# Kernel optimization log

Measured on AMD Instinct MI355X. Metric: run time of the kernel, lower is better.

Reference implementation:

```python
import jax, jax.numpy as jnp
import numpy as np

B, S, E = 4, 4096, 512
H, D = 8, 64
BS = 64
R = 3
FF = 2048
N = S // BS
NEG = -10000.0


def _ln(x, g, b):
    m = jnp.mean(x, -1, keepdims=True)
    v = jnp.mean((x - m) ** 2, -1, keepdims=True)
    return (x - m) * jax.lax.rsqrt(v + 1e-6) * g + b


def setup_inputs():
    key = jax.random.key(0)
    k = jax.random.split(key, 8)
    s = 0.02
    return {
        "inputs": jax.random.normal(k[0], (B, S, E), jnp.float32),
        "band_mask": jnp.ones((B, 1, N - 4, BS, 3 * BS), jnp.float32),
        "from_mask": jnp.ones((B, 1, S, 1), jnp.float32),
        "to_mask": jnp.ones((B, 1, 1, S), jnp.float32),
        "blocked_mask": jnp.ones((B, N, BS), jnp.float32),
        "Wq": jax.random.normal(k[1], (E, H, D), jnp.float32) * s,
        "bq": jnp.zeros((H, D), jnp.float32),
        "Wk": jax.random.normal(k[2], (E, H, D), jnp.float32) * s,
        "bk": jnp.zeros((H, D), jnp.float32),
        "Wv": jax.random.normal(k[3], (E, H, D), jnp.float32) * s,
        "bv": jnp.zeros((H, D), jnp.float32),
        "Wo": jax.random.normal(k[4], (H, D, E), jnp.float32) * s,
        "bo": jnp.zeros((E,), jnp.float32),
        "W1": jax.random.normal(k[5], (E, FF), jnp.float32) * s,
        "b1": jnp.zeros((FF,), jnp.float32),
        "W2": jax.random.normal(k[6], (FF, E), jnp.float32) * s,
        "b2": jnp.zeros((E,), jnp.float32),
        "g1": jnp.ones((E,), jnp.float32),
        "beta1": jnp.zeros((E,), jnp.float32),
        "g2": jnp.ones((E,), jnp.float32),
        "beta2": jnp.zeros((E,), jnp.float32),
        "rand_attn": jax.random.randint(k[7], (H, N - 2, R), 0, N, jnp.int32),
    }


def _forward(inputs, band_mask, from_mask, to_mask, blocked_mask, Wq, bq, Wk, bk, Wv, bv, Wo, bo, W1, b1, W2, b2, g1, beta1, g2, beta2, rand_attn):
    b, s, e = inputs.shape
    h, d = Wq.shape[1], Wq.shape[2]
    bs = blocked_mask.shape[2]
    n = s // bs
    r = rand_attn.shape[2]
    scale = d ** -0.5
    # qkv projections (Dense3d): [b,s,e] -> [b,h,s,d]
    q = jnp.einsum("bse,ehd->bhsd", inputs, Wq) + bq[None, :, None, :]
    kmat = jnp.einsum("bse,ehd->bhsd", inputs, Wk) + bk[None, :, None, :]
    vmat = jnp.einsum("bse,ehd->bhsd", inputs, Wv) + bv[None, :, None, :]
    qb = q.reshape(b, h, n, bs, d)
    kb = kmat.reshape(b, h, n, bs, d)
    vb = vmat.reshape(b, h, n, bs, d)
    # gather per-head random key/value blocks: [b,h,n-2,r*bs,d]
    hidx = jnp.arange(h)[:, None, None]
    gk = kb[:, hidx, rand_attn].reshape(b, h, n - 2, r * bs, d)
    gv = vb[:, hidx, rand_attn].reshape(b, h, n - 2, r * bs, d)
    gm = blocked_mask[:, rand_attn].reshape(b, h, n - 2, r * bs)
    rand_mask = jnp.einsum("blq,bhlk->bhlqk", blocked_mask[:, 1:-1], gm)
    # first query block: dense attention over all keys
    fp = jnp.einsum("bhqd,bhkd->bhqk", qb[:, :, 0], kmat) * scale + (1.0 - to_mask) * NEG
    fc = jnp.einsum("bhqk,bhkd->bhqd", jax.nn.softmax(fp, -1), vmat)
    # second query block: blocks [0,1,2,-1] + random blocks of row 1
    skm = jnp.concatenate([kb[:, :, 0], kb[:, :, 1], kb[:, :, 2], kb[:, :, -1], gk[:, :, 0]], 2)
    svm = jnp.concatenate([vb[:, :, 0], vb[:, :, 1], vb[:, :, 2], vb[:, :, -1], gv[:, :, 0]], 2)
    seq_pad = jnp.concatenate([to_mask[:, :, :, :3 * bs], to_mask[:, :, :, -bs:], jnp.ones((b, 1, 1, r * bs), to_mask.dtype)], 3)
    rand_pad = jnp.concatenate([jnp.ones((b, h, bs, 4 * bs), rand_mask.dtype), rand_mask[:, :, 0]], 3)
    sp = jnp.einsum("bhqd,bhkd->bhqk", qb[:, :, 1], skm) * scale + (1.0 - jnp.minimum(seq_pad, rand_pad)) * NEG
    sc = jnp.einsum("bhqk,bhkd->bhqd", jax.nn.softmax(sp, -1), svm)
    # middle blocks: sliding 3-block band + random + global first/last blocks
    mq = qb[:, :, 2:-2]  # [b,h,n-4,bs,d]
    ekm = jnp.concatenate([kb[:, :, 1:-3], kb[:, :, 2:-2], kb[:, :, 3:-1]], 3)  # [b,h,n-4,3bs,d]
    evm = jnp.concatenate([vb[:, :, 1:-3], vb[:, :, 2:-2], vb[:, :, 3:-1]], 3)
    inner = jnp.einsum("bhlqd,bhlkd->bhlqk", mq, ekm) * scale + (1.0 - band_mask) * NEG
    rbp = jnp.einsum("bhlqd,bhlkd->bhlqk", mq, gk[:, :, 1:-1]) * scale + (1.0 - rand_mask[:, :, 1:-1]) * NEG
    fbp = jnp.einsum("bhlqd,bhkd->bhlqk", mq, kb[:, :, 0]) * scale + (1.0 - to_mask[:, :, None, :, :bs]) * NEG
    lbp = jnp.einsum("bhlqd,bhkd->bhlqk", mq, kb[:, :, -1]) * scale + (1.0 - to_mask[:, :, None, :, -bs:]) * NEG
    ba = jax.nn.softmax(jnp.concatenate([fbp, inner, rbp, lbp], -1), -1)
    mc = (jnp.einsum("bhlqk,bhlkd->bhlqd", ba[..., bs:4 * bs], evm)
          + jnp.einsum("bhlqk,bhlkd->bhlqd", ba[..., 4 * bs:(4 + r) * bs], gv[:, :, 1:-1])
          + jnp.einsum("bhlqk,bhkd->bhlqd", ba[..., :bs], vb[:, :, 0])
          + jnp.einsum("bhlqk,bhkd->bhlqd", ba[..., -bs:], vb[:, :, -1]))
    # second-to-last query block
    slkm = jnp.concatenate([kb[:, :, 0], kb[:, :, -3], kb[:, :, -2], kb[:, :, -1], gk[:, :, -1]], 2)
    slvm = jnp.concatenate([vb[:, :, 0], vb[:, :, -3], vb[:, :, -2], vb[:, :, -1], gv[:, :, -1]], 2)
    sl_seq = jnp.concatenate([to_mask[:, :, :, :bs], to_mask[:, :, :, -3 * bs:], jnp.ones((b, 1, 1, r * bs), to_mask.dtype)], 3)
    sl_rand = jnp.concatenate([jnp.ones((b, h, bs, 4 * bs), rand_mask.dtype), rand_mask[:, :, -1]], 3)
    slp = jnp.einsum("bhqd,bhkd->bhqk", qb[:, :, -2], slkm) * scale + (1.0 - jnp.minimum(sl_seq, sl_rand)) * NEG
    slc = jnp.einsum("bhqk,bhkd->bhqd", jax.nn.softmax(slp, -1), slvm)
    # last query block: dense over all keys
    lp = jnp.einsum("bhqd,bhkd->bhqk", qb[:, :, -1], kmat) * scale + (1.0 - to_mask) * NEG
    lc = jnp.einsum("bhqk,bhkd->bhqd", jax.nn.softmax(lp, -1), vmat)
    ctx = jnp.concatenate([fc[:, :, None], sc[:, :, None], mc, slc[:, :, None], lc[:, :, None]], 2)
    ctx = ctx.reshape(b, h, s, d) * from_mask
    ctx = ctx.transpose(0, 2, 1, 3)  # [b,s,h,d]
    attn_out = jnp.einsum("bshd,hde->bse", ctx, Wo) + bo
    out1 = _ln(inputs + attn_out, g1, beta1)
    ffn = jnp.maximum(out1 @ W1 + b1, 0.0) @ W2 + b2
    return _ln(out1 + ffn, g2, beta2)


def reference(inputs, band_mask, from_mask, to_mask, blocked_mask, Wq, bq, Wk, bk, Wv, bv, Wo, bo, W1, b1, W2, b2, g1, beta1, g2, beta2, rand_attn):
    return _forward(inputs, band_mask, from_mask, to_mask, blocked_mask, Wq, bq, Wk, bk, Wv, bv, Wo, bo, W1, b1, W2, b2, g1, beta1, g2, beta2, rand_attn)
```

## Files before the change

### kernel.cpp

```cpp
#include <hip/hip_runtime.h>
#include <hip/hip_bf16.h>

typedef __bf16 bf16x8 __attribute__((ext_vector_type(8)));
typedef float f32x4 __attribute__((ext_vector_type(4)));

static constexpr size_t MB = 1024 * 1024;

__device__ __forceinline__ void gload16(const void* g, void* l) {
  __builtin_amdgcn_global_load_lds((const __attribute__((address_space(1))) unsigned int*)g,
                                   (__attribute__((address_space(3))) unsigned int*)l,
                                   16, 0, 0);
}

__device__ __forceinline__ unsigned short f2b(float x) {
  union { __hip_bfloat16 h; unsigned short u; } cv;
  cv.h = __float2bfloat16(x);
  return cv.u;
}

__global__ __launch_bounds__(256) void pack_k(
    const float* __restrict__ X,
    const float* __restrict__ Wq, const float* __restrict__ Wk, const float* __restrict__ Wv,
    const float* __restrict__ Wo, const float* __restrict__ W1, const float* __restrict__ W2,
    __hip_bfloat16* __restrict__ XB, __hip_bfloat16* __restrict__ WQKVT,
    __hip_bfloat16* __restrict__ WOT, __hip_bfloat16* __restrict__ W1T,
    __hip_bfloat16* __restrict__ W2T)
{
  unsigned int i = blockIdx.x * 256u + threadIdx.x;
  if (i < 8388608u) { XB[i] = __float2bfloat16(X[i]); return; }
  i -= 8388608u;
  if (i < 786432u) {
    unsigned int n = i >> 9, k = i & 511u, which = n >> 9, hd = n & 511u;
    const float* W = (which == 0) ? Wq : (which == 1) ? Wk : Wv;
    WQKVT[i] = __float2bfloat16(W[k * 512u + hd]);
    return;
  }
  i -= 786432u;
  if (i < 262144u) {
    unsigned int e = i >> 9, hd = i & 511u;
    WOT[i] = __float2bfloat16(Wo[hd * 512u + e]);
    return;
  }
  i -= 262144u;
  if (i < 1048576u) {
    unsigned int f = i >> 9, e = i & 511u;
    W1T[i] = __float2bfloat16(W1[e * 2048u + f]);
    return;
  }
  i -= 1048576u;
  {
    unsigned int e = i >> 11, f = i & 2047u;
    W2T[i] = __float2bfloat16(W2[f * 512u + e]);
  }
}

template<int EPI>
__global__ __launch_bounds__(256) void gemm_k(
    const __hip_bfloat16* __restrict__ A,
    const __hip_bfloat16* __restrict__ Bt,
    int M, int N, int K,
    const float* __restrict__ bias0, const float* __restrict__ bias1, const float* __restrict__ bias2,
    void* __restrict__ o0, void* __restrict__ o1, void* __restrict__ o2)
{
  __shared__ __align__(16) char lA[128 * 64 * 2];
  __shared__ __align__(16) char lB[128 * 64 * 2];
  const int tid = threadIdx.x;
  const int wv = tid >> 6, ln = tid & 63;
  const int g = ln >> 4, q16 = ln & 15;
  const int mT = M >> 7;
  const int bm = blockIdx.x % mT, bn = blockIdx.x / mT;
  const int row0 = bm << 7, col0 = bn << 7;
  const int wm = wv >> 1, wn = wv & 1;
  const int ktn = K >> 6;

  f32x4 acc[4][4] = {};

  for (int kt = 0; kt < ktn; ++kt) {
    #pragma unroll
    for (int c4 = 0; c4 < 4; ++c4) {
      int c = wv * 4 + c4;
      int o = c * 1024 + ln * 16;
      int r = o >> 7;
      int slot = (o >> 4) & 7;
      int koff = kt * 64 + ((slot ^ (r & 7)) << 3);
      gload16(A + (size_t)(row0 + r) * K + koff, lA + c * 1024);
      gload16(Bt + (size_t)(col0 + r) * K + koff, lB + c * 1024);
    }
    __syncthreads();
    #pragma unroll
    for (int ks = 0; ks < 2; ++ks) {
      bf16x8 af[4], bfr[4];
      #pragma unroll
      for (int m = 0; m < 4; ++m) {
        int r = wm * 64 + m * 16 + q16;
        af[m] = *(const bf16x8*)(lA + r * 128 + (((4 * ks + g) ^ (r & 7)) << 4));
      }
      #pragma unroll
      for (int n = 0; n < 4; ++n) {
        int r = wn * 64 + n * 16 + q16;
        bfr[n] = *(const bf16x8*)(lB + r * 128 + (((4 * ks + g) ^ (r & 7)) << 4));
      }
      #pragma unroll
      for (int m = 0; m < 4; ++m) {
        #pragma unroll
        for (int n = 0; n < 4; ++n) {
          acc[m][n] = __builtin_amdgcn_mfma_f32_16x16x32_bf16(af[m], bfr[n], acc[m][n], 0, 0, 0);
        }
      }
    }
    __syncthreads();
  }

  #pragma unroll
  for (int m = 0; m < 4; ++m) {
    int rowb = row0 + wm * 64 + m * 16 + g * 4;
    #pragma unroll
    for (int n = 0; n < 4; ++n) {
      int col = col0 + wn * 64 + n * 16 + q16;
      f32x4 v = acc[m][n];
      if constexpr (EPI == 0) {
        int which = col >> 9, hd = col & 511;
        int hh = hd >> 6, dd = hd & 63;
        float bb = ((which == 0) ? bias0 : (which == 1) ? bias1 : bias2)[hd];
        if (which == 2) {
          int b_ = rowb >> 12, s0 = rowb & 4095;
          unsigned int lo = (unsigned)f2b(v[0] + bb) | ((unsigned)f2b(v[1] + bb) << 16);
          unsigned int hi = (unsigned)f2b(v[2] + bb) | ((unsigned)f2b(v[3] + bb) << 16);
          uint2 pv; pv.x = lo; pv.y = hi;
          *(uint2*)((char*)o2 + (((size_t)(b_ * 8 + hh) * 64 + dd) * 4096 + s0) * 2) = pv;
        } else {
          __hip_bfloat16* base = (__hip_bfloat16*)((which == 0) ? o0 : o1);
          #pragma unroll
          for (int r = 0; r < 4; ++r) {
            int rowg = rowb + r;
            int b_ = rowg >> 12, s = rowg & 4095;
            base[((size_t)(b_ * 8 + hh) * 4096 + s) * 64 + dd] = __float2bfloat16(v[r] + bb);
          }
        }
      } else {
        float bb = bias0[col];
        __hip_bfloat16* O = (__hip_bfloat16*)o0;
        #pragma unroll
        for (int r = 0; r < 4; ++r) {
          float x = v[r] + bb;
          if constexpr (EPI == 2) x = fmaxf(x, 0.f);
          O[(size_t)(rowb + r) * N + col] = __float2bfloat16(x);
        }
      }
    }
  }
}

#define NMID 1984
__global__ __launch_bounds__(256) void attn_k(
    const __hip_bfloat16* __restrict__ QB,
    const __hip_bfloat16* __restrict__ KB,
    const __hip_bfloat16* __restrict__ VT,
    const int* __restrict__ rand_attn,
    __hip_bfloat16* __restrict__ CTX,
    float* __restrict__ EOT,
    float* __restrict__ EML)
{
  __shared__ __align__(16) char lK[4][8192];
  __shared__ __align__(16) char lV[4][8192];
  __shared__ __align__(16) char lP[4][2816];

  const int tid = threadIdx.x;
  const int wv = tid >> 6, ln = tid & 63;
  const int g = ln >> 4, q16 = ln & 15;

  const bool edge = (int)blockIdx.x >= NMID;
  int bh, l, nk, split = 0, chunk = 0;
  int r0 = 0, r1 = 0, r2 = 0;
  if (!edge) {
    bh = blockIdx.x / 62;
    l = 1 + blockIdx.x % 62;
    nk = (l == 1 || l == 62) ? 7 : 8;
    const int* rp = rand_attn + ((bh & 7) * 62 + (l - 1)) * 3;
    r0 = rp[0]; r1 = rp[1]; r2 = rp[2];
  } else {
    chunk = (int)blockIdx.x - NMID;
    split = chunk & 7;
    int be = chunk >> 3;
    bh = be >> 1;
    l = (be & 1) ? 63 : 0;
    nk = 8;
  }

  auto kbof = [&](int t) -> int {
    if (edge) return split * 8 + t;
    if (t == 0) return 0;
    if (t >= 4) return (t == 4) ? r0 : (t == 5) ? r1 : (t == 6) ? r2 : 63;
    if (l == 1) return (t == 3) ? 63 : t;
    return l - 2 + t;
  };

  const __hip_bfloat16* Kbase = KB + ((size_t)bh << 18);
  const __hip_bfloat16* Vbase = VT + ((size_t)bh << 18);

  auto stage = [&](int t) {
    int kb = kbof(t);
    char* dK = lK[t & 3];
    char* dV = lV[t & 3];
    #pragma unroll
    for (int cc = 0; cc < 2; ++cc) {
      int c = wv * 2 + cc;
      int o = c * 1024 + ln * 16;
      int r = o >> 7;
      int slot = (o >> 4) & 7;
      int sw8 = (slot ^ (r & 7)) << 3;
      gload16(Kbase + ((size_t)(kb * 64 + r) << 6) + sw8, dK + c * 1024);
      gload16(Vbase + ((size_t)r << 12) + kb * 64 + sw8, dV + c * 1024);
    }
  };

  const size_t sq = (size_t)bh * 4096 + l * 64 + wv * 16 + q16;
  bf16x8 qreg0 = *(const bf16x8*)(QB + sq * 64 + g * 8);
  bf16x8 qreg1 = *(const bf16x8*)(QB + sq * 64 + 32 + g * 8);

  f32x4 ot[4] = {};
  float l_part = 0.f;
  constexpr float C = 0.18033688011112042f;

  auto compute = [&](int t) {
    const char* bK = lK[t & 3];
    const char* bV = lV[t & 3];
    f32x4 st[4];
    #pragma unroll
    for (int m = 0; m < 4; ++m) {
      int r = m * 16 + q16;
      bf16x8 kf0 = *(const bf16x8*)(bK + r * 128 + ((g ^ (r & 7)) << 4));
      bf16x8 kf1 = *(const bf16x8*)(bK + r * 128 + (((4 + g) ^ (r & 7)) << 4));
      f32x4 z = {};
      st[m] = __builtin_amdgcn_mfma_f32_16x16x32_bf16(kf0, qreg0, z, 0, 0, 0);
      st[m] = __builtin_amdgcn_mfma_f32_16x16x32_bf16(kf1, qreg1, st[m], 0, 0, 0);
    }
    #pragma unroll
    for (int m = 0; m < 4; ++m) {
      #pragma unroll
      for (int r = 0; r < 4; ++r) {
        float p = __builtin_amdgcn_exp2f(st[m][r] * C);
        st[m][r] = p;
        l_part += p;
      }
    }
    #pragma unroll
    for (int m = 0; m < 4; ++m) {
      unsigned int lo = (unsigned)f2b(st[m][0]) | ((unsigned)f2b(st[m][1]) << 16);
      unsigned int hi = (unsigned)f2b(st[m][2]) | ((unsigned)f2b(st[m][3]) << 16);
      uint2 pv; pv.x = lo; pv.y = hi;
      *(uint2*)(lP[wv] + q16 * 176 + 32 * m + 8 * g) = pv;
    }
    asm volatile("s_waitcnt lgkmcnt(0)" ::: "memory");
    __builtin_amdgcn_sched_barrier(0);
    #pragma unroll
    for (int ks = 0; ks < 2; ++ks) {
      bf16x8 pb = *(const bf16x8*)(lP[wv] + q16 * 176 + 64 * ks + 16 * g);
      #pragma unroll
      for (int m = 0; m < 4; ++m) {
        int r = m * 16 + q16;
        bf16x8 vf = *(const bf16x8*)(bV + r * 128 + (((4 * ks + g) ^ (r & 7)) << 4));
        ot[m] = __builtin_amdgcn_mfma_f32_16x16x32_bf16(vf, pb, ot[m], 0, 0, 0);
      }
    }
  };

  stage(0); stage(1); stage(2);

  int t = 0;
  for (; t + 3 < nk; ++t) {
    asm volatile("s_waitcnt vmcnt(8)" ::: "memory");
    __builtin_amdgcn_s_barrier();
    __builtin_amdgcn_sched_barrier(0);
    stage(t + 3);
    compute(t);
  }
  asm volatile("s_waitcnt vmcnt(8)" ::: "memory");
  __builtin_amdgcn_s_barrier();
  __builtin_amdgcn_sched_barrier(0);
  compute(t); ++t;
  asm volatile("s_waitcnt vmcnt(4)" ::: "memory");
  __builtin_amdgcn_s_barrier();
  __builtin_amdgcn_sched_barrier(0);
  compute(t); ++t;
  asm volatile("s_waitcnt vmcnt(0)" ::: "memory");
  __builtin_amdgcn_s_barrier();
  __builtin_amdgcn_sched_barrier(0);
  compute(t);

  float lsum = l_part;
  lsum += __shfl_xor(lsum, 16);
  lsum += __shfl_xor(lsum, 32);

  if (!edge) {
    int b = bh >> 3, h = bh & 7;
    float inv = 1.f / lsum;
    size_t crow = ((size_t)b * 4096 + l * 64 + wv * 16 + q16) * 512 + h * 64;
    #pragma unroll
    for (int m = 0; m < 4; ++m) {
      int d0 = 16 * m + 4 * g;
      unsigned int lo = (unsigned)f2b(ot[m][0] * inv) | ((unsigned)f2b(ot[m][1] * inv) << 16);
      unsigned int hi = (unsigned)f2b(ot[m][2] * inv) | ((unsigned)f2b(ot[m][3] * inv) << 16);
      uint2 pv; pv.x = lo; pv.y = hi;
      *(uint2*)((char*)CTX + (crow + d0) * 2) = pv;
    }
  } else {
    int qg = wv * 16 + q16;
    float* O = EOT + (size_t)chunk * 4096;
    #pragma unroll
    for (int m = 0; m < 4; ++m) {
      #pragma unroll
      for (int r = 0; r < 4; ++r)
        O[(16 * m + 4 * g + r) * 64 + qg] = ot[m][r];
    }
    if (g == 0) EML[(size_t)chunk * 64 + qg] = lsum;
  }
}

__global__ __launch_bounds__(256) void attn_combine_k(
    const float* __restrict__ EOT, const float* __restrict__ EML,
    __hip_bfloat16* __restrict__ CTX)
{
  const int be = blockIdx.x;
  const int bh = be >> 1, e = be & 1, b = bh >> 3, h = bh & 7;
  const int q = threadIdx.x & 63, dgrp = threadIdx.x >> 6;

  float denom = 0.f;
  #pragma unroll
  for (int s = 0; s < 8; ++s) denom += EML[(size_t)(be * 8 + s) * 64 + q];
  float inv = 1.f / denom;

  const size_t srow = (size_t)b * 4096 + (e ? 4032 : 0) + q;
  #pragma unroll
  for (int dd = 0; dd < 16; ++dd) {
    int d = dgrp * 16 + dd;
    float acc = 0.f;
    #pragma unroll
    for (int s = 0; s < 8; ++s)
      acc += EOT[(size_t)(be * 8 + s) * 4096 + d * 64 + q];
    CTX[srow * 512 + h * 64 + d] = __float2bfloat16(acc * inv);
  }
}

template<typename TX, typename TY, bool OUTF>
__global__ __launch_bounds__(256) void ln_k(
    const TX* __restrict__ X, const TY* __restrict__ Y,
    const float* __restrict__ gamma, const float* __restrict__ beta,
    float* __restrict__ outF, __hip_bfloat16* __restrict__ outB)
{
  const int wv = threadIdx.x >> 6, ln = threadIdx.x & 63;
  const size_t row = (size_t)blockIdx.x * 4 + wv;
  float v[8];
  {
    const TX* xr = X + row * 512 + ln * 8;
    const TY* yr = Y + row * 512 + ln * 8;
    if constexpr (sizeof(TX) == 4) {
      float4 a0 = *(const float4*)xr, a1 = *(const float4*)(xr + 4);
      v[0]=a0.x; v[1]=a0.y; v[2]=a0.z; v[3]=a0.w; v[4]=a1.x; v[5]=a1.y; v[6]=a1.z; v[7]=a1.w;
    } else {
      bf16x8 a = *(const bf16x8*)xr;
      #pragma unroll
      for (int i = 0; i < 8; ++i) v[i] = (float)a[i];
    }
    if constexpr (sizeof(TY) == 4) {
      float4 b0 = *(const float4*)yr, b1 = *(const float4*)(yr + 4);
      v[0]+=b0.x; v[1]+=b0.y; v[2]+=b0.z; v[3]+=b0.w; v[4]+=b1.x; v[5]+=b1.y; v[6]+=b1.z; v[7]+=b1.w;
    } else {
      bf16x8 bv_ = *(const bf16x8*)yr;
      #pragma unroll
      for (int i = 0; i < 8; ++i) v[i] += (float)bv_[i];
    }
  }
  float s = 0.f;
  #pragma unroll
  for (int i = 0; i < 8; ++i) s += v[i];
  #pragma unroll
  for (int o = 1; o < 64; o <<= 1) s += __shfl_xor(s, o);
  float mean = s * (1.f / 512.f);
  float sq = 0.f;
  #pragma unroll
  for (int i = 0; i < 8; ++i) { float d = v[i] - mean; sq += d * d; }
  #pragma unroll
  for (int o = 1; o < 64; o <<= 1) sq += __shfl_xor(sq, o);
  float rs = rsqrtf(sq * (1.f / 512.f) + 1e-6f);
  float og[8];
  #pragma unroll
  for (int i = 0; i < 8; ++i)
    og[i] = (v[i] - mean) * rs * gamma[ln * 8 + i] + beta[ln * 8 + i];
  if constexpr (OUTF) {
    float4 o0; o0.x = og[0]; o0.y = og[1]; o0.z = og[2]; o0.w = og[3];
    float4 o1; o1.x = og[4]; o1.y = og[5]; o1.z = og[6]; o1.w = og[7];
    *(float4*)(outF + row * 512 + ln * 8) = o0;
    *(float4*)(outF + row * 512 + ln * 8 + 4) = o1;
  } else {
    unsigned int w0 = (unsigned)f2b(og[0]) | ((unsigned)f2b(og[1]) << 16);
    unsigned int w1 = (unsigned)f2b(og[2]) | ((unsigned)f2b(og[3]) << 16);
    unsigned int w2 = (unsigned)f2b(og[4]) | ((unsigned)f2b(og[5]) << 16);
    unsigned int w3 = (unsigned)f2b(og[6]) | ((unsigned)f2b(og[7]) << 16);
    uint2 p0; p0.x = w0; p0.y = w1;
    uint2 p1; p1.x = w2; p1.y = w3;
    *(uint2*)((char*)outB + (row * 512 + ln * 8) * 2) = p0;
    *(uint2*)((char*)outB + (row * 512 + ln * 8 + 4) * 2) = p1;
  }
}

extern "C" void kernel_launch(void* const* d_in, const int* in_sizes, int n_in,
                              void* d_out, int out_size, void* d_ws, size_t ws_size,
                              hipStream_t stream)
{
  (void)in_sizes; (void)n_in; (void)out_size; (void)ws_size;
  const float* X   = (const float*)d_in[0];
  const float* Wq  = (const float*)d_in[5];
  const float* bq  = (const float*)d_in[6];
  const float* Wk  = (const float*)d_in[7];
  const float* bk  = (const float*)d_in[8];
  const float* Wv  = (const float*)d_in[9];
  const float* bv  = (const float*)d_in[10];
  const float* Wo  = (const float*)d_in[11];
  const float* bo  = (const float*)d_in[12];
  const float* W1  = (const float*)d_in[13];
  const float* b1  = (const float*)d_in[14];
  const float* W2  = (const float*)d_in[15];
  const float* b2  = (const float*)d_in[16];
  const float* g1  = (const float*)d_in[17];
  const float* be1 = (const float*)d_in[18];
  const float* g2  = (const float*)d_in[19];
  const float* be2 = (const float*)d_in[20];
  const int*   ra  = (const int*)d_in[21];

  char* ws = (char*)d_ws;
  __hip_bfloat16* WQKVT = (__hip_bfloat16*)(ws + 0 * MB);
  __hip_bfloat16* WOT   = (__hip_bfloat16*)(ws + 2 * MB);
  __hip_bfloat16* W1T   = (__hip_bfloat16*)(ws + 3 * MB);
  __hip_bfloat16* W2T   = (__hip_bfloat16*)(ws + 5 * MB);
  __hip_bfloat16* XB    = (__hip_bfloat16*)(ws + 8 * MB);
  float*          EOT   = (float*)(ws + 8 * MB);
  float*          EML   = (float*)(ws + 16 * MB);
  __hip_bfloat16* QB    = (__hip_bfloat16*)(ws + 24 * MB);
  __hip_bfloat16* KBp   = (__hip_bfloat16*)(ws + 40 * MB);
  __hip_bfloat16* VTp   = (__hip_bfloat16*)(ws + 56 * MB);
  __hip_bfloat16* CTX   = (__hip_bfloat16*)(ws + 72 * MB);
  __hip_bfloat16* AOB   = (__hip_bfloat16*)(ws + 88 * MB);
  __hip_bfloat16* O1B   = (__hip_bfloat16*)(ws + 104 * MB);
  __hip_bfloat16* F2B   = (__hip_bfloat16*)(ws + 120 * MB);
  __hip_bfloat16* H1    = (__hip_bfloat16*)(ws + 24 * MB);

  pack_k<<<dim3(45056), dim3(256), 0, stream>>>(X, Wq, Wk, Wv, Wo, W1, W2,
                                                XB, WQKVT, WOT, W1T, W2T);
  gemm_k<0><<<dim3(128 * 12), dim3(256), 0, stream>>>(XB, WQKVT, 16384, 1536, 512,
                                                      bq, bk, bv, QB, KBp, VTp);
  attn_k<<<dim3(NMID + 512), dim3(256), 0, stream>>>(QB, KBp, VTp, ra, CTX, EOT, EML);
  attn_combine_k<<<dim3(64), dim3(256), 0, stream>>>(EOT, EML, CTX);
  gemm_k<1><<<dim3(128 * 4), dim3(256), 0, stream>>>(CTX, WOT, 16384, 512, 512,
                                                     bo, nullptr, nullptr, AOB, nullptr, nullptr);
  ln_k<float, __hip_bfloat16, false><<<dim3(4096), dim3(256), 0, stream>>>(
      X, AOB, g1, be1, nullptr, O1B);
  gemm_k<2><<<dim3(128 * 16), dim3(256), 0, stream>>>(O1B, W1T, 16384, 2048, 512,
                                                      b1, nullptr, nullptr, H1, nullptr, nullptr);
  gemm_k<1><<<dim3(128 * 4), dim3(256), 0, stream>>>(H1, W2T, 16384, 512, 2048,
                                                     b2, nullptr, nullptr, F2B, nullptr, nullptr);
  ln_k<__hip_bfloat16, __hip_bfloat16, true><<<dim3(4096), dim3(256), 0, stream>>>(
      O1B, F2B, g2, be2, (float*)d_out, nullptr);
}
```

Measured before the change: 264.3 us.

## Tile-transpose weight packing and split attention keys across two wave groups

The pack kernel now converts X with vectorized 8-element loads and stores, and transposes the weights through a shared-memory 64x64 tile so that both reads and writes are coalesced. The attention kernel doubles its block to 512 threads. Two wave groups each handle half of the key rows of every 64-key block, and their partial outputs and row sums are reduced through LDS at the end. The K/V pipeline drops from four buffers to two, waiting on vmcnt(0) each step. This trades load prefetch depth for more waves per block and adds an extra barrier plus an LDS reduction.

```diff
diff --git a/kernel.cpp b/kernel.cpp
--- a/kernel.cpp
+++ b/kernel.cpp
@@ -18,7 +18,7 @@
   return cv.u;
 }
 
-__global__ __launch_bounds__(256) void pack_k(
+__global__ __launch_bounds__(256) void pt_k(
     const float* __restrict__ X,
     const float* __restrict__ Wq, const float* __restrict__ Wk, const float* __restrict__ Wv,
     const float* __restrict__ Wo, const float* __restrict__ W1, const float* __restrict__ W2,
@@ -26,31 +26,41 @@
     __hip_bfloat16* __restrict__ WOT, __hip_bfloat16* __restrict__ W1T,
     __hip_bfloat16* __restrict__ W2T)
 {
-  unsigned int i = blockIdx.x * 256u + threadIdx.x;
-  if (i < 8388608u) { XB[i] = __float2bfloat16(X[i]); return; }
-  i -= 8388608u;
-  if (i < 786432u) {
-    unsigned int n = i >> 9, k = i & 511u, which = n >> 9, hd = n & 511u;
-    const float* W = (which == 0) ? Wq : (which == 1) ? Wk : Wv;
-    WQKVT[i] = __float2bfloat16(W[k * 512u + hd]);
+  __shared__ float tile[64][65];
+  const int bid = blockIdx.x, tid = threadIdx.x;
+  if (bid < 4096) {
+    size_t i = (size_t)bid * 2048 + tid * 8;
+    float4 a0 = *(const float4*)(X + i);
+    float4 a1 = *(const float4*)(X + i + 4);
+    unsigned int w0 = (unsigned)f2b(a0.x) | ((unsigned)f2b(a0.y) << 16);
+    unsigned int w1 = (unsigned)f2b(a0.z) | ((unsigned)f2b(a0.w) << 16);
+    unsigned int w2 = (unsigned)f2b(a1.x) | ((unsigned)f2b(a1.y) << 16);
+    unsigned int w3 = (unsigned)f2b(a1.z) | ((unsigned)f2b(a1.w) << 16);
+    uint4 p; p.x = w0; p.y = w1; p.z = w2; p.w = w3;
+    *(uint4*)(XB + i) = p;
     return;
   }
-  i -= 786432u;
-  if (i < 262144u) {
-    unsigned int e = i >> 9, hd = i & 511u;
-    WOT[i] = __float2bfloat16(Wo[hd * 512u + e]);
-    return;
-  }
-  i -= 262144u;
-  if (i < 1048576u) {
-    unsigned int f = i >> 9, e = i & 511u;
-    W1T[i] = __float2bfloat16(W1[e * 2048u + f]);
-    return;
-  }
-  i -= 1048576u;
-  {
-    unsigned int e = i >> 11, f = i & 2047u;
-    W2T[i] = __float2bfloat16(W2[f * 512u + e]);
+  int tb = bid - 4096;
+  const float* in; __hip_bfloat16* out; int R, C, tt;
+  if (tb < 64)       { in = Wq; out = WQKVT;          R = 512;  C = 512;  tt = tb; }
+  else if (tb < 128) { in = Wk; out = WQKVT + 262144; R = 512;  C = 512;  tt = tb - 64; }
+  else if (tb < 192) { in = Wv; out = WQKVT + 524288; R = 512;  C = 512;  tt = tb - 128; }
+  else if (tb < 256) { in = Wo; out = WOT;            R = 512;  C = 512;  tt = tb - 192; }
+  else if (tb < 512) { in = W1; out = W1T;            R = 512;  C = 2048; tt = tb - 256; }
+  else               { in = W2; out = W2T;            R = 2048; C = 512;  tt = tb - 512; }
+  const int ct = C >> 6;
+  const int r0 = (tt / ct) << 6, c0 = (tt % ct) << 6;
+  const int tx = tid & 63, ty = tid >> 6;
+  #pragma unroll
+  for (int j = 0; j < 16; ++j) {
+    int r = ty * 16 + j;
+    tile[r][tx] = in[(size_t)(r0 + r) * C + c0 + tx];
+  }
+  __syncthreads();
+  #pragma unroll
+  for (int j = 0; j < 16; ++j) {
+    int c = ty * 16 + j;
+    out[(size_t)(c0 + c) * R + r0 + tx] = __float2bfloat16(tile[tx][c]);
   }
 }
 
@@ -152,7 +162,7 @@
 }
 
 #define NMID 1984
-__global__ __launch_bounds__(256) void attn_k(
+__global__ __launch_bounds__(512) void attn_k(
     const __hip_bfloat16* __restrict__ QB,
     const __hip_bfloat16* __restrict__ KB,
     const __hip_bfloat16* __restrict__ VT,
@@ -161,13 +171,14 @@
     float* __restrict__ EOT,
     float* __restrict__ EML)
 {
-  __shared__ __align__(16) char lK[4][8192];
-  __shared__ __align__(16) char lV[4][8192];
+  __shared__ __align__(16) char lK[2][8192];
+  __shared__ __align__(16) char lV[2][8192];
   __shared__ __align__(16) char lP[4][2816];
 
   const int tid = threadIdx.x;
   const int wv = tid >> 6, ln = tid & 63;
   const int g = ln >> 4, q16 = ln & 15;
+  const int kh = wv >> 2, qg = wv & 3;
 
   const bool edge = (int)blockIdx.x >= NMID;
   int bh, l, nk, split = 0, chunk = 0;
@@ -200,21 +211,14 @@
 
   auto stage = [&](int t) {
     int kb = kbof(t);
-    char* dK = lK[t & 3];
-    char* dV = lV[t & 3];
-    #pragma unroll
-    for (int cc = 0; cc < 2; ++cc) {
-      int c = wv * 2 + cc;
-      int o = c * 1024 + ln * 16;
-      int r = o >> 7;
-      int slot = (o >> 4) & 7;
-      int sw8 = (slot ^ (r & 7)) << 3;
-      gload16(Kbase + ((size_t)(kb * 64 + r) << 6) + sw8, dK + c * 1024);
-      gload16(Vbase + ((size_t)r << 12) + kb * 64 + sw8, dV + c * 1024);
-    }
+    int o = wv * 1024 + ln * 16;
+    int r = o >> 7;
+    int sw8 = ((ln & 7) ^ (r & 7)) << 3;
+    gload16(Kbase + ((size_t)(kb * 64 + r) << 6) + sw8, lK[t & 1] + wv * 1024);
+    gload16(Vbase + ((size_t)r << 12) + kb * 64 + sw8, lV[t & 1] + wv * 1024);
   };
 
-  const size_t sq = (size_t)bh * 4096 + l * 64 + wv * 16 + q16;
+  const size_t sq = (size_t)bh * 4096 + l * 64 + qg * 16 + q16;
   bf16x8 qreg0 = *(const bf16x8*)(QB + sq * 64 + g * 8);
   bf16x8 qreg1 = *(const bf16x8*)(QB + sq * 64 + 32 + g * 8);
 
@@ -223,97 +227,103 @@
   constexpr float C = 0.18033688011112042f;
 
   auto compute = [&](int t) {
-    const char* bK = lK[t & 3];
-    const char* bV = lV[t & 3];
-    f32x4 st[4];
-    #pragma unroll
-    for (int m = 0; m < 4; ++m) {
+    const char* bK = lK[t & 1];
+    const char* bV = lV[t & 1];
+    f32x4 st[2];
+    #pragma unroll
+    for (int j = 0; j < 2; ++j) {
+      int m = 2 * kh + j;
       int r = m * 16 + q16;
       bf16x8 kf0 = *(const bf16x8*)(bK + r * 128 + ((g ^ (r & 7)) << 4));
       bf16x8 kf1 = *(const bf16x8*)(bK + r * 128 + (((4 + g) ^ (r & 7)) << 4));
       f32x4 z = {};
-      st[m] = __builtin_amdgcn_mfma_f32_16x16x32_bf16(kf0, qreg0, z, 0, 0, 0);
-      st[m] = __builtin_amdgcn_mfma_f32_16x16x32_bf16(kf1, qreg1, st[m], 0, 0, 0);
-    }
-    #pragma unroll
-    for (int m = 0; m < 4; ++m) {
+      st[j] = __builtin_amdgcn_mfma_f32_16x16x32_bf16(kf0, qreg0, z, 0, 0, 0);
+      st[j] = __builtin_amdgcn_mfma_f32_16x16x32_bf16(kf1, qreg1, st[j], 0, 0, 0);
+    }
+    #pragma unroll
+    for (int j = 0; j < 2; ++j) {
       #pragma unroll
       for (int r = 0; r < 4; ++r) {
-        float p = __builtin_amdgcn_exp2f(st[m][r] * C);
-        st[m][r] = p;
+        float p = __builtin_amdgcn_exp2f(st[j][r] * C);
+        st[j][r] = p;
         l_part += p;
       }
     }
     #pragma unroll
-    for (int m = 0; m < 4; ++m) {
-      unsigned int lo = (unsigned)f2b(st[m][0]) | ((unsigned)f2b(st[m][1]) << 16);
-      unsigned int hi = (unsigned)f2b(st[m][2]) | ((unsigned)f2b(st[m][3]) << 16);
+    for (int j = 0; j < 2; ++j) {
+      int m = 2 * kh + j;
+      unsigned int lo = (unsigned)f2b(st[j][0]) | ((unsigned)f2b(st[j][1]) << 16);
+      unsigned int hi = (unsigned)f2b(st[j][2]) | ((unsigned)f2b(st[j][3]) << 16);
       uint2 pv; pv.x = lo; pv.y = hi;
-      *(uint2*)(lP[wv] + q16 * 176 + 32 * m + 8 * g) = pv;
+      *(uint2*)(lP[qg] + q16 * 176 + 32 * m + 8 * g) = pv;
     }
     asm volatile("s_waitcnt lgkmcnt(0)" ::: "memory");
     __builtin_amdgcn_sched_barrier(0);
-    #pragma unroll
-    for (int ks = 0; ks < 2; ++ks) {
-      bf16x8 pb = *(const bf16x8*)(lP[wv] + q16 * 176 + 64 * ks + 16 * g);
-      #pragma unroll
-      for (int m = 0; m < 4; ++m) {
-        int r = m * 16 + q16;
-        bf16x8 vf = *(const bf16x8*)(bV + r * 128 + (((4 * ks + g) ^ (r & 7)) << 4));
-        ot[m] = __builtin_amdgcn_mfma_f32_16x16x32_bf16(vf, pb, ot[m], 0, 0, 0);
-      }
+    bf16x8 pb = *(const bf16x8*)(lP[qg] + q16 * 176 + 64 * kh + 16 * g);
+    #pragma unroll
+    for (int m = 0; m < 4; ++m) {
+      int r = m * 16 + q16;
+      bf16x8 vf = *(const bf16x8*)(bV + r * 128 + (((4 * kh + g) ^ (r & 7)) << 4));
+      ot[m] = __builtin_amdgcn_mfma_f32_16x16x32_bf16(vf, pb, ot[m], 0, 0, 0);
     }
   };
 
-  stage(0); stage(1); stage(2);
-
-  int t = 0;
-  for (; t + 3 < nk; ++t) {
-    asm volatile("s_waitcnt vmcnt(8)" ::: "memory");
+  stage(0);
+  for (int t = 0; t < nk; ++t) {
+    asm volatile("s_waitcnt vmcnt(0)" ::: "memory");
     __builtin_amdgcn_s_barrier();
     __builtin_amdgcn_sched_barrier(0);
-    stage(t + 3);
+    if (t + 1 < nk) stage(t + 1);
     compute(t);
   }
-  asm volatile("s_waitcnt vmcnt(8)" ::: "memory");
-  __builtin_amdgcn_s_barrier();
-  __builtin_amdgcn_sched_barrier(0);
-  compute(t); ++t;
-  asm volatile("s_waitcnt vmcnt(4)" ::: "memory");
-  __builtin_amdgcn_s_barrier();
-  __builtin_amdgcn_sched_barrier(0);
-  compute(t); ++t;
-  asm volatile("s_waitcnt vmcnt(0)" ::: "memory");
-  __builtin_amdgcn_s_barrier();
-  __builtin_amdgcn_sched_barrier(0);
-  compute(t);
 
   float lsum = l_part;
   lsum += __shfl_xor(lsum, 16);
   lsum += __shfl_xor(lsum, 32);
 
-  if (!edge) {
-    int b = bh >> 3, h = bh & 7;
-    float inv = 1.f / lsum;
-    size_t crow = ((size_t)b * 4096 + l * 64 + wv * 16 + q16) * 512 + h * 64;
-    #pragma unroll
-    for (int m = 0; m < 4; ++m) {
-      int d0 = 16 * m + 4 * g;
-      unsigned int lo = (unsigned)f2b(ot[m][0] * inv) | ((unsigned)f2b(ot[m][1] * inv) << 16);
-      unsigned int hi = (unsigned)f2b(ot[m][2] * inv) | ((unsigned)f2b(ot[m][3] * inv) << 16);
-      uint2 pv; pv.x = lo; pv.y = hi;
-      *(uint2*)((char*)CTX + (crow + d0) * 2) = pv;
-    }
-  } else {
-    int qg = wv * 16 + q16;
-    float* O = EOT + (size_t)chunk * 4096;
-    #pragma unroll
-    for (int m = 0; m < 4; ++m) {
+  __builtin_amdgcn_s_barrier();
+  float* red = (float*)lK;
+  float* lre = (float*)lV;
+  const int lane256 = qg * 64 + ln;
+  if (kh == 1) {
+    #pragma unroll
+    for (int m = 0; m < 4; ++m)
       #pragma unroll
       for (int r = 0; r < 4; ++r)
-        O[(16 * m + 4 * g + r) * 64 + qg] = ot[m][r];
-    }
-    if (g == 0) EML[(size_t)chunk * 64 + qg] = lsum;
+        red[(4 * m + r) * 256 + lane256] = ot[m][r];
+    lre[lane256] = lsum;
+  }
+  __syncthreads();
+  if (kh == 0) {
+    #pragma unroll
+    for (int m = 0; m < 4; ++m)
+      #pragma unroll
+      for (int r = 0; r < 4; ++r)
+        ot[m][r] += red[(4 * m + r) * 256 + lane256];
+    lsum += lre[lane256];
+
+    if (!edge) {
+      int b = bh >> 3, h = bh & 7;
+      float inv = 1.f / lsum;
+      size_t crow = ((size_t)b * 4096 + l * 64 + qg * 16 + q16) * 512 + h * 64;
+      #pragma unroll
+      for (int m = 0; m < 4; ++m) {
+        int d0 = 16 * m + 4 * g;
+        unsigned int lo = (unsigned)f2b(ot[m][0] * inv) | ((unsigned)f2b(ot[m][1] * inv) << 16);
+        unsigned int hi = (unsigned)f2b(ot[m][2] * inv) | ((unsigned)f2b(ot[m][3] * inv) << 16);
+        uint2 pv; pv.x = lo; pv.y = hi;
+        *(uint2*)((char*)CTX + (crow + d0) * 2) = pv;
+      }
+    } else {
+      int qgl = qg * 16 + q16;
+      float* O = EOT + (size_t)chunk * 4096;
+      #pragma unroll
+      for (int m = 0; m < 4; ++m)
+        #pragma unroll
+        for (int r = 0; r < 4; ++r)
+          O[(16 * m + 4 * g + r) * 64 + qgl] = ot[m][r];
+      if (g == 0) EML[(size_t)chunk * 64 + qgl] = lsum;
+    }
   }
 }
 
@@ -445,11 +455,11 @@
   __hip_bfloat16* F2B   = (__hip_bfloat16*)(ws + 120 * MB);
   __hip_bfloat16* H1    = (__hip_bfloat16*)(ws + 24 * MB);
 
-  pack_k<<<dim3(45056), dim3(256), 0, stream>>>(X, Wq, Wk, Wv, Wo, W1, W2,
-                                                XB, WQKVT, WOT, W1T, W2T);
+  pt_k<<<dim3(4864), dim3(256), 0, stream>>>(X, Wq, Wk, Wv, Wo, W1, W2,
+                                             XB, WQKVT, WOT, W1T, W2T);
   gemm_k<0><<<dim3(128 * 12), dim3(256), 0, stream>>>(XB, WQKVT, 16384, 1536, 512,
                                                       bq, bk, bv, QB, KBp, VTp);
-  attn_k<<<dim3(NMID + 512), dim3(256), 0, stream>>>(QB, KBp, VTp, ra, CTX, EOT, EML);
+  attn_k<<<dim3(NMID + 512), dim3(512), 0, stream>>>(QB, KBp, VTp, ra, CTX, EOT, EML);
   attn_combine_k<<<dim3(64), dim3(256), 0, stream>>>(EOT, EML, CTX);
   gemm_k<1><<<dim3(128 * 4), dim3(256), 0, stream>>>(CTX, WOT, 16384, 512, 512,
                                                      bo, nullptr, nullptr, AOB, nullptr, nullptr);
```

Result: faster. 241.6 us (-8.6%).
